# Kernel optimization log

Hardware: AMD Instinct MI355X
Metric: run time of the kernel (lower is better)

## Reference

```python
import jax, jax.numpy as jnp
import numpy as np

N = 20000      # num nodes
E = 320000     # num edges (before self loops)
DIN = 128      # in_channels
DH = 128       # hidden channels
C = 40         # num classes


def setup_inputs() -> dict:
    key = jax.random.key(0)
    ks = jax.random.split(key, 16)
    s_in = 1.0 / np.sqrt(DIN)
    s_h = 1.0 / np.sqrt(DH)
    s_a = 1.0 / np.sqrt(2 * DH)
    return {
        "x": jax.random.normal(ks[0], (N, DIN), jnp.float32),
        "edge_index": jax.random.randint(ks[1], (2, E), 0, N),
        "norm": jax.random.uniform(ks[2], (E + N,), jnp.float32),  # Jaccard sims in [0,1]
        # layer 1 params
        "W1": jax.random.uniform(ks[3], (DIN, DH), jnp.float32, -s_in, s_in),
        "aW1": jax.random.uniform(ks[4], (2 * DH, 1), jnp.float32, -s_a, s_a),
        "ab1": jax.random.uniform(ks[5], (1,), jnp.float32, -s_a, s_a),
        "alpha1": jnp.array([0.5], jnp.float32),
        "b1": jnp.zeros((DH,), jnp.float32),
        # layer 2 params
        "W2": jax.random.uniform(ks[6], (DH, DH), jnp.float32, -s_h, s_h),
        "aW2": jax.random.uniform(ks[7], (2 * DH, 1), jnp.float32, -s_a, s_a),
        "ab2": jax.random.uniform(ks[8], (1,), jnp.float32, -s_a, s_a),
        "alpha2": jnp.array([0.5], jnp.float32),
        "b2": jnp.zeros((DH,), jnp.float32),
        # output head
        "Wout": jax.random.uniform(ks[9], (DH, C), jnp.float32, -s_h, s_h),
        "bout": jax.random.uniform(ks[10], (C,), jnp.float32, -s_h, s_h),
    }


def _gat_layer(x, src, dst, norm, W, aW, ab, alpha, bias):
    n = x.shape[0]
    h = x @ W                              # [N, DH]
    s = h[src]                             # gathered source feats [E', DH]
    t = h[dst]                             # gathered target feats [E', DH]
    # attention logit per edge -> exp(leaky_relu(.))
    e = jnp.exp(jax.nn.leaky_relu(jnp.concatenate([s, t], axis=-1) @ aW + ab,
                                  negative_slope=0.2))          # [E', 1]
    e_sum = jax.ops.segment_sum(e, dst, num_segments=n)         # softmax denom per dst node
    a = e / e_sum[dst]
    s_sim = jnp.exp(norm)[:, None]                               # [E', 1]
    s_sum = jax.ops.segment_sum(s_sim, src, num_segments=n)     # note: summed over SRC (as in original)
    sw = s_sim / s_sum[dst]                                      # but indexed by DST (as in original)
    al = jnp.clip(alpha, 1e-4, 0.9999)
    w = al * a + (1.0 - al) * sw                                 # blended edge weight [E', 1]
    out = jax.ops.segment_max(w * s, dst, num_segments=n)        # aggr='max' propagate
    return out + bias


def reference(x, edge_index, norm, W1, aW1, ab1, alpha1, b1,
              W2, aW2, ab2, alpha2, b2, Wout, bout):
    n = x.shape[0]
    loops = jnp.arange(n, dtype=edge_index.dtype)
    src = jnp.concatenate([edge_index[0], loops])   # add_self_loops
    dst = jnp.concatenate([edge_index[1], loops])
    h = jax.nn.relu(_gat_layer(x, src, dst, norm, W1, aW1, ab1, alpha1, b1))
    h = jax.nn.relu(_gat_layer(h, src, dst, norm, W2, aW2, ab2, alpha2, b2))
    return jax.nn.log_softmax(h @ Wout + bout, axis=-1)
```

## Files before the change

kernel.cpp:

```cpp
#include <hip/hip_runtime.h>
#include <math.h>

#define DHID 128
#define NCLS 40
#define ELLW 64

typedef unsigned int   u32;
typedef unsigned short u16;
using short8 = __attribute__((ext_vector_type(8))) short;
using f32x4  = __attribute__((ext_vector_type(4))) float;

__device__ __forceinline__ u16 f2bf(float f) {
  u32 u = __float_as_uint(f);
  return (u16)((u + 0x7FFFu + ((u >> 16) & 1u)) >> 16);
}
__device__ __forceinline__ float bf_lo(u32 p) { return __uint_as_float(p << 16); }
__device__ __forceinline__ float bf_hi(u32 p) { return __uint_as_float(p & 0xFFFF0000u); }

__global__ __launch_bounds__(256) void prep_kernel(
    const float* __restrict__ x, const float* __restrict__ W1,
    const float* __restrict__ W2, u16* __restrict__ xbf,
    u16* __restrict__ Wp1, u16* __restrict__ Wp2,
    int* __restrict__ counts, float* __restrict__ ssum,
    int* __restrict__ ovf_cnt, int N) {
  int gi = blockIdx.x * 256 + threadIdx.x;
  int Ncvt = N * 16;
  if (gi < Ncvt) {
    int base = gi * 8;
    float4 v0 = *reinterpret_cast<const float4*>(x + base);
    float4 v1 = *reinterpret_cast<const float4*>(x + base + 4);
    uint4 o;
    o.x = (u32)f2bf(v0.x) | ((u32)f2bf(v0.y) << 16);
    o.y = (u32)f2bf(v0.z) | ((u32)f2bf(v0.w) << 16);
    o.z = (u32)f2bf(v1.x) | ((u32)f2bf(v1.y) << 16);
    o.w = (u32)f2bf(v1.z) | ((u32)f2bf(v1.w) << 16);
    *reinterpret_cast<uint4*>(xbf + base) = o;
    return;
  }
  gi -= Ncvt;
  if (gi < N) { counts[gi] = 0; ssum[gi] = 0.f; return; }
  gi -= N;
  if (gi < 32768) {
    int layer = gi >> 14, q = gi & 16383;
    int j = q & 7, l = (q >> 3) & 63, kt = (q >> 9) & 3, ct = q >> 11;
    int k = kt * 32 + (l >> 4) * 8 + j;
    int col = ct * 16 + (l & 15);
    const float* Wsrc = layer ? W2 : W1;
    u16* Wdst = layer ? Wp2 : Wp1;
    Wdst[q] = f2bf(Wsrc[k * DHID + col]);
    return;
  }
  gi -= 32768;
  if (gi == 0) *ovf_cnt = 0;
}

__device__ __forceinline__ void mfma_gemm_block(
    float* Cl, float* P, const u16* __restrict__ Xbf,
    const u16* __restrict__ Wp, const float* __restrict__ aW,
    u16* __restrict__ Hout, float* __restrict__ elo, float* __restrict__ ero,
    int n, int rowBase) {
  int t = threadIdx.x;
  int w = t >> 6, l = t & 63;
  int lr = l & 15, lh = l >> 4;
  f32x4 acc00 = {0.f,0.f,0.f,0.f}, acc01 = {0.f,0.f,0.f,0.f};
  f32x4 acc10 = {0.f,0.f,0.f,0.f}, acc11 = {0.f,0.f,0.f,0.f};
  int r0 = rowBase + lr;      if (r0 > n - 1) r0 = n - 1;
  int r1 = rowBase + 16 + lr; if (r1 > n - 1) r1 = n - 1;
  const u16* a0p = Xbf + (size_t)r0 * DHID;
  const u16* a1p = Xbf + (size_t)r1 * DHID;
  const u16* wb0 = Wp + ((size_t)(w * 2 + 0) * 4 * 64 + l) * 8;
  const u16* wb1 = Wp + ((size_t)(w * 2 + 1) * 4 * 64 + l) * 8;
#pragma unroll
  for (int kt = 0; kt < 4; ++kt) {
    int ko = kt * 32 + lh * 8;
    short8 fa0 = *reinterpret_cast<const short8*>(a0p + ko);
    short8 fa1 = *reinterpret_cast<const short8*>(a1p + ko);
    short8 fb0 = *reinterpret_cast<const short8*>(wb0 + kt * 64 * 8);
    short8 fb1 = *reinterpret_cast<const short8*>(wb1 + kt * 64 * 8);
    acc00 = __builtin_amdgcn_mfma_f32_16x16x32_bf16(fa0, fb0, acc00, 0, 0, 0);
    acc01 = __builtin_amdgcn_mfma_f32_16x16x32_bf16(fa0, fb1, acc01, 0, 0, 0);
    acc10 = __builtin_amdgcn_mfma_f32_16x16x32_bf16(fa1, fb0, acc10, 0, 0, 0);
    acc11 = __builtin_amdgcn_mfma_f32_16x16x32_bf16(fa1, fb1, acc11, 0, 0, 0);
  }
#pragma unroll
  for (int j = 0; j < 4; ++j) {
    Cl[(lh * 4 + j) * DHID + w * 32 + lr]           = acc00[j];
    Cl[(lh * 4 + j) * DHID + w * 32 + 16 + lr]      = acc01[j];
    Cl[(16 + lh * 4 + j) * DHID + w * 32 + lr]      = acc10[j];
    Cl[(16 + lh * 4 + j) * DHID + w * 32 + 16 + lr] = acc11[j];
  }
  __syncthreads();
  int r = t >> 3, cg = (t & 7) * 16;
  const float* crow = Cl + r * DHID + cg;
  float pl = 0.f, pr = 0.f;
  int gr = rowBase + r;
  u32 packed[4];
#pragma unroll
  for (int q = 0; q < 4; ++q) {
    float v0 = crow[q * 4 + 0], v1 = crow[q * 4 + 1];
    float v2 = crow[q * 4 + 2], v3 = crow[q * 4 + 3];
    pl = fmaf(v0, aW[cg + q * 4 + 0], pl); pr = fmaf(v0, aW[DHID + cg + q * 4 + 0], pr);
    pl = fmaf(v1, aW[cg + q * 4 + 1], pl); pr = fmaf(v1, aW[DHID + cg + q * 4 + 1], pr);
    pl = fmaf(v2, aW[cg + q * 4 + 2], pl); pr = fmaf(v2, aW[DHID + cg + q * 4 + 2], pr);
    pl = fmaf(v3, aW[cg + q * 4 + 3], pl); pr = fmaf(v3, aW[DHID + cg + q * 4 + 3], pr);
    packed[q] = (u32)f2bf(v0) | ((u32)f2bf(v1) << 16) |
                0;
    packed[q] |= 0;
  }
  if (gr < n) {
    uint4 o;
    o.x = (u32)f2bf(crow[0])  | ((u32)f2bf(crow[1])  << 16);
    o.y = (u32)f2bf(crow[2])  | ((u32)f2bf(crow[3])  << 16);
    o.z = (u32)f2bf(crow[4])  | ((u32)f2bf(crow[5])  << 16);
    o.w = (u32)f2bf(crow[6])  | ((u32)f2bf(crow[7])  << 16);
    *reinterpret_cast<uint4*>(Hout + (size_t)gr * DHID + cg) = o;
    uint4 o2;
    o2.x = (u32)f2bf(crow[8])  | ((u32)f2bf(crow[9])  << 16);
    o2.y = (u32)f2bf(crow[10]) | ((u32)f2bf(crow[11]) << 16);
    o2.z = (u32)f2bf(crow[12]) | ((u32)f2bf(crow[13]) << 16);
    o2.w = (u32)f2bf(crow[14]) | ((u32)f2bf(crow[15]) << 16);
    *reinterpret_cast<uint4*>(Hout + (size_t)gr * DHID + cg + 8) = o2;
  }
  P[r * 16 + (t & 7) * 2 + 0] = pl;
  P[r * 16 + (t & 7) * 2 + 1] = pr;
  __syncthreads();
  if (t < 64) {
    int half = t >> 5, rr = t & 31;
    float s = 0.f;
#pragma unroll
    for (int cq = 0; cq < 8; ++cq) s += P[rr * 16 + cq * 2 + half];
    int g2 = rowBase + rr;
    if (g2 < n) { if (half) ero[g2] = s; else elo[g2] = s; }
  }
}

__global__ __launch_bounds__(256) void gemm1_build_kernel(
    const u16* __restrict__ Xbf, const u16* __restrict__ Wp,
    const float* __restrict__ aW, u16* __restrict__ H,
    float* __restrict__ el, float* __restrict__ er, int n, int gT,
    const int* __restrict__ ei, const float* __restrict__ norm,
    int* __restrict__ counts, float* __restrict__ ssum,
    uint2* __restrict__ ell, uint4* __restrict__ ovf,
    int* __restrict__ ovf_cnt, int E, int EP) {
  __shared__ float Cl[32 * DHID];
  __shared__ float P[32 * 16];
  if (blockIdx.x < gT) {
    mfma_gemm_block(Cl, P, Xbf, Wp, aW, H, el, er, n, blockIdx.x * 32);
  } else {
    int k = (blockIdx.x - gT) * 256 + threadIdx.x;
    if (k < EP) {
      int src, dst;
      if (k < E) { src = ei[k]; dst = ei[E + k]; }
      else       { src = dst = k - E; }
      float se = __expf(norm[k]);
      atomicAdd(&ssum[src], se);
      int slot = atomicAdd(&counts[dst], 1);
      if (slot < ELLW) {
        ell[(size_t)dst * ELLW + slot] =
            make_uint2((u32)src, __float_as_uint(se));
      } else {
        int o = atomicAdd(ovf_cnt, 1);
        ovf[o] = make_uint4((u32)dst, (u32)src, __float_as_uint(se), 0u);
      }
    }
  }
}

__global__ __launch_bounds__(256) void gemm_elr_kernel(
    const u16* __restrict__ Xbf, const u16* __restrict__ Wp,
    const float* __restrict__ aW, u16* __restrict__ H,
    float* __restrict__ el, float* __restrict__ er, int n) {
  __shared__ float Cl[32 * DHID];
  __shared__ float P[32 * 16];
  mfma_gemm_block(Cl, P, Xbf, Wp, aW, H, el, er, n, blockIdx.x * 32);
}

__device__ __forceinline__ void agg_node8(
    const u16* __restrict__ H, const int* __restrict__ counts,
    const uint2* __restrict__ ell, const uint4* __restrict__ ovf, int ovfN,
    const float* __restrict__ el, const float* __restrict__ ssum,
    float base, float al, int node, int lane, float a[8]) {
  int deg = counts[node];
  int dell = deg < ELLW ? deg : ELLW;
  const uint2* erow = ell + (size_t)node * ELLW;
  int src0 = 0; float sx0 = 0.f;
  if (lane < dell) {
    uint2 rec = erow[lane];
    src0 = (int)rec.x;
    sx0  = __uint_as_float(rec.y);
  }
  int qw = lane >> 4;
  const u16* Hf = H + ((lane & 15) << 3);
  int ei0 = qw, ei1 = 4 + qw;
  int ci0 = ei0 < dell ? ei0 : 0;
  int ci1 = ei1 < dell ? ei1 : 0;
  int ps0 = __shfl(src0, ci0);
  int ps1 = __shfl(src0, ci1);
  uint4 pr0 = *reinterpret_cast<const uint4*>(Hf + (size_t)ps0 * DHID);
  uint4 pr1 = *reinterpret_cast<const uint4*>(Hf + (size_t)ps1 * DHID);
  float e0 = 0.f;
  if (lane < dell) {
    float g = el[src0] + base;
    e0 = __expf(g > 0.f ? g : 0.2f * g);
  }
  float es = e0;
  if (ovfN > 0 && deg > ELLW) {
    for (int cb = 0; cb < ovfN; cb += 64) {
      int i = cb + lane;
      if (i < ovfN) {
        uint4 r = ovf[i];
        if ((int)r.x == node) {
          float g = el[(int)r.y] + base;
          es += __expf(g > 0.f ? g : 0.2f * g);
        }
      }
    }
  }
#pragma unroll
  for (int off = 32; off; off >>= 1) es += __shfl_xor(es, off);
  float invEs = al / es;
  float omaS  = (1.f - al) / ssum[node];
  float w0 = e0 * invEs + sx0 * omaS;
#pragma unroll
  for (int i = 0; i < 8; ++i) a[i] = -INFINITY;
  {
    float wA = __shfl(w0, ci0);
    float wB = __shfl(w0, ci1);
    if (ei0 < dell) {
      a[0] = fmaxf(a[0], wA * bf_lo(pr0.x)); a[1] = fmaxf(a[1], wA * bf_hi(pr0.x));
      a[2] = fmaxf(a[2], wA * bf_lo(pr0.y)); a[3] = fmaxf(a[3], wA * bf_hi(pr0.y));
      a[4] = fmaxf(a[4], wA * bf_lo(pr0.z)); a[5] = fmaxf(a[5], wA * bf_hi(pr0.z));
      a[6] = fmaxf(a[6], wA * bf_lo(pr0.w)); a[7] = fmaxf(a[7], wA * bf_hi(pr0.w));
    }
    if (ei1 < dell) {
      a[0] = fmaxf(a[0], wB * bf_lo(pr1.x)); a[1] = fmaxf(a[1], wB * bf_hi(pr1.x));
      a[2] = fmaxf(a[2], wB * bf_lo(pr1.y)); a[3] = fmaxf(a[3], wB * bf_hi(pr1.y));
      a[4] = fmaxf(a[4], wB * bf_lo(pr1.z)); a[5] = fmaxf(a[5], wB * bf_hi(pr1.z));
      a[6] = fmaxf(a[6], wB * bf_lo(pr1.w)); a[7] = fmaxf(a[7], wB * bf_hi(pr1.w));
    }
  }
  int j = 8;
  for (; j + 7 < dell; j += 8) {
    int ea = j + qw, eb = j + 4 + qw;
    int   sa = __shfl(src0, ea); float wa = __shfl(w0, ea);
    int   sb = __shfl(src0, eb); float wb = __shfl(w0, eb);
    uint4 ha = *reinterpret_cast<const uint4*>(Hf + (size_t)sa * DHID);
    uint4 hb = *reinterpret_cast<const uint4*>(Hf + (size_t)sb * DHID);
    a[0] = fmaxf(a[0], fmaxf(wa * bf_lo(ha.x), wb * bf_lo(hb.x)));
    a[1] = fmaxf(a[1], fmaxf(wa * bf_hi(ha.x), wb * bf_hi(hb.x)));
    a[2] = fmaxf(a[2], fmaxf(wa * bf_lo(ha.y), wb * bf_lo(hb.y)));
    a[3] = fmaxf(a[3], fmaxf(wa * bf_hi(ha.y), wb * bf_hi(hb.y)));
    a[4] = fmaxf(a[4], fmaxf(wa * bf_lo(ha.z), wb * bf_lo(hb.z)));
    a[5] = fmaxf(a[5], fmaxf(wa * bf_hi(ha.z), wb * bf_hi(hb.z)));
    a[6] = fmaxf(a[6], fmaxf(wa * bf_lo(ha.w), wb * bf_lo(hb.w)));
    a[7] = fmaxf(a[7], fmaxf(wa * bf_hi(ha.w), wb * bf_hi(hb.w)));
  }
  for (; j < dell; j += 4) {
    int e = j + qw;
    int ec = e < dell ? e : dell - 1;
    int   sa = __shfl(src0, ec); float wa = __shfl(w0, ec);
    if (e < dell) {
      uint4 ha = *reinterpret_cast<const uint4*>(Hf + (size_t)sa * DHID);
      a[0] = fmaxf(a[0], wa * bf_lo(ha.x));
      a[1] = fmaxf(a[1], wa * bf_hi(ha.x));
      a[2] = fmaxf(a[2], wa * bf_lo(ha.y));
      a[3] = fmaxf(a[3], wa * bf_hi(ha.y));
      a[4] = fmaxf(a[4], wa * bf_lo(ha.z));
      a[5] = fmaxf(a[5], wa * bf_hi(ha.z));
      a[6] = fmaxf(a[6], wa * bf_lo(ha.w));
      a[7] = fmaxf(a[7], wa * bf_hi(ha.w));
    }
  }
  if (ovfN > 0 && deg > ELLW) {
    for (int cb = 0; cb < ovfN; cb += 64) {
      int i = cb + lane;
      uint4 r = (i < ovfN) ? ovf[i] : make_uint4(0u, 0u, 0u, 0u);
      bool match = (i < ovfN) && ((int)r.x == node);
      int si = (int)r.y;
      float wi = 0.f;
      if (match) {
        float g = el[si] + base;
        wi = __expf(g > 0.f ? g : 0.2f * g) * invEs +
             __uint_as_float(r.z) * omaS;
      }
      unsigned long long mask = __ballot(match);
      while (mask) {
        int jb = __ffsll(mask) - 1;
        mask &= mask - 1;
        int   sj = __shfl(si, jb);
        float wj = __shfl(wi, jb);
        uint4 h = *reinterpret_cast<const uint4*>(Hf + (size_t)sj * DHID);
        a[0] = fmaxf(a[0], wj * bf_lo(h.x)); a[1] = fmaxf(a[1], wj * bf_hi(h.x));
        a[2] = fmaxf(a[2], wj * bf_lo(h.y)); a[3] = fmaxf(a[3], wj * bf_hi(h.y));
        a[4] = fmaxf(a[4], wj * bf_lo(h.z)); a[5] = fmaxf(a[5], wj * bf_hi(h.z));
        a[6] = fmaxf(a[6], wj * bf_lo(h.w)); a[7] = fmaxf(a[7], wj * bf_hi(h.w));
      }
    }
  }
#pragma unroll
  for (int i = 0; i < 8; ++i) {
    a[i] = fmaxf(a[i], __shfl_xor(a[i], 16));
    a[i] = fmaxf(a[i], __shfl_xor(a[i], 32));
  }
}

__global__ __launch_bounds__(256) void agg_kernel(
    const u16* __restrict__ H, const int* __restrict__ counts,
    const uint2* __restrict__ ell, const uint4* __restrict__ ovf,
    const int* __restrict__ ovf_cnt, const float* __restrict__ el,
    const float* __restrict__ er, const float* __restrict__ ssum,
    const float* __restrict__ ab, const float* __restrict__ alpha,
    const float* __restrict__ bias, u16* __restrict__ Y, int n) {
  int node = blockIdx.x * 4 + (threadIdx.x >> 6);
  int lane = threadIdx.x & 63;
  if (node >= n) return;
  int ovfN = *ovf_cnt;
  float al = fminf(fmaxf(alpha[0], 1e-4f), 0.9999f);
  float base = er[node] + ab[0];
  float a[8];
  agg_node8(H, counts, ell, ovf, ovfN, el, ssum, base, al, node, lane, a);
  if (lane < 16) {
    int fl = lane << 3;
    float v[8];
#pragma unroll
    for (int i = 0; i < 8; ++i) v[i] = fmaxf(a[i] + bias[fl + i], 0.f);
    uint4 o;
    o.x = (u32)f2bf(v[0]) | ((u32)f2bf(v[1]) << 16);
    o.y = (u32)f2bf(v[2]) | ((u32)f2bf(v[3]) << 16);
    o.z = (u32)f2bf(v[4]) | ((u32)f2bf(v[5]) << 16);
    o.w = (u32)f2bf(v[6]) | ((u32)f2bf(v[7]) << 16);
    *reinterpret_cast<uint4*>(Y + (size_t)node * DHID + fl) = o;
  }
}

__global__ __launch_bounds__(256) void agg_head_kernel(
    const u16* __restrict__ H, const int* __restrict__ counts,
    const uint2* __restrict__ ell, const uint4* __restrict__ ovf,
    const int* __restrict__ ovf_cnt, const float* __restrict__ el,
    const float* __restrict__ er, const float* __restrict__ ssum,
    const float* __restrict__ ab, const float* __restrict__ alpha,
    const float* __restrict__ bias, const float* __restrict__ Wout,
    const float* __restrict__ bout, float* __restrict__ out, int n) {
  __shared__ float Wl[DHID * NCLS];
  __shared__ float hl[4][DHID];
  int t = threadIdx.x;
  for (int i = t; i < DHID * NCLS; i += 256) Wl[i] = Wout[i];
  int wv = t >> 6, lane = t & 63;
  int node = blockIdx.x * 4 + wv;
  if (node < n) {
    int ovfN = *ovf_cnt;
    float al = fminf(fmaxf(alpha[0], 1e-4f), 0.9999f);
    float base = er[node] + ab[0];
    float a[8];
    agg_node8(H, counts, ell, ovf, ovfN, el, ssum, base, al, node, lane, a);
    if (lane < 16) {
      int fl = lane << 3;
#pragma unroll
      for (int i = 0; i < 8; ++i)
        hl[wv][fl + i] = fmaxf(a[i] + bias[fl + i], 0.f);
    }
  }
  __syncthreads();
  if (node >= n) return;
  float z = -INFINITY;
  bool act = lane < NCLS;
  if (act) {
    z = bout[lane];
    const float* hr = hl[wv];
#pragma unroll 8
    for (int k = 0; k < DHID; ++k) z = fmaf(hr[k], Wl[k * NCLS + lane], z);
  }
  float m = z;
#pragma unroll
  for (int off = 32; off; off >>= 1) m = fmaxf(m, __shfl_xor(m, off));
  float p = act ? expf(z - m) : 0.f;
#pragma unroll
  for (int off = 32; off; off >>= 1) p += __shfl_xor(p, off);
  float ls = logf(p);
  if (act) out[(size_t)node * NCLS + lane] = z - m - ls;
}

extern "C" void kernel_launch(void* const* d_in, const int* in_sizes, int n_in,
                              void* d_out, int out_size, void* d_ws, size_t ws_size,
                              hipStream_t stream) {
  const float* x     = (const float*)d_in[0];
  const int*   ei    = (const int*)d_in[1];
  const float* norm  = (const float*)d_in[2];
  const float* W1    = (const float*)d_in[3];
  const float* aW1   = (const float*)d_in[4];
  const float* ab1   = (const float*)d_in[5];
  const float* alpha1= (const float*)d_in[6];
  const float* b1    = (const float*)d_in[7];
  const float* W2    = (const float*)d_in[8];
  const float* aW2   = (const float*)d_in[9];
  const float* ab2   = (const float*)d_in[10];
  const float* alpha2= (const float*)d_in[11];
  const float* b2    = (const float*)d_in[12];
  const float* Wout  = (const float*)d_in[13];
  const float* bout  = (const float*)d_in[14];
  float* out = (float*)d_out;

  const int N  = in_sizes[0] / DHID;
  const int E  = in_sizes[1] / 2;
  const int EP = E + N;

  char* ws = (char*)d_ws;
  size_t off = 0;
  auto alloc = [&](size_t bytes) -> void* {
    void* p = ws + off;
    off += (bytes + 255) & ~(size_t)255;
    return p;
  };
  int*   counts  = (int*)  alloc((size_t)N * 4);
  float* ssum    = (float*)alloc((size_t)N * 4);
  int*   ovf_cnt = (int*)  alloc(256);
  u16*   xbf     = (u16*)  alloc((size_t)N * DHID * 2);
  u16*   Wp1     = (u16*)  alloc(16384 * 2);
  u16*   Wp2     = (u16*)  alloc(16384 * 2);
  u16*   Hbf     = (u16*)  alloc((size_t)N * DHID * 2);
  u16*   Bbf     = (u16*)  alloc((size_t)N * DHID * 2);
  float* el      = (float*)alloc((size_t)N * 4);
  float* er      = (float*)alloc((size_t)N * 4);
  uint2* ell     = (uint2*)alloc((size_t)N * ELLW * 8);
  uint4* ovf     = (uint4*)alloc((size_t)EP * 16);

  const int gEdge = (EP + 255) / 256;
  const int gT    = (N + 31) / 32;
  const int gAgg  = (N + 3) / 4;
  const int prepWork = N * 16 + N + 32768 + 1;
  const int gPrep = (prepWork + 255) / 256;

  prep_kernel<<<gPrep, 256, 0, stream>>>(x, W1, W2, xbf, Wp1, Wp2,
                                         counts, ssum, ovf_cnt, N);
  gemm1_build_kernel<<<gT + gEdge, 256, 0, stream>>>(
      xbf, Wp1, aW1, Hbf, el, er, N, gT, ei, norm, counts, ssum, ell, ovf,
      ovf_cnt, E, EP);
  agg_kernel<<<gAgg, 256, 0, stream>>>(Hbf, counts, ell, ovf, ovf_cnt, el, er,
                                       ssum, ab1, alpha1, b1, Bbf, N);
  gemm_elr_kernel<<<gT, 256, 0, stream>>>(Bbf, Wp2, aW2, Hbf, el, er, N);
  agg_head_kernel<<<gAgg, 256, 0, stream>>>(Hbf, counts, ell, ovf, ovf_cnt,
                                            el, er, ssum, ab2, alpha2, b2,
                                            Wout, bout, out, N);
}
```

Measured before the change: 104.7 us.

## Fuse all stages into one cooperative persistent kernel with grid syncs

```diff
diff --git a/kernel.cpp b/kernel.cpp
--- a/kernel.cpp
+++ b/kernel.cpp
@@ -1,9 +1,12 @@
 #include <hip/hip_runtime.h>
+#include <hip/hip_cooperative_groups.h>
 #include <math.h>
 
 #define DHID 128
 #define NCLS 40
 #define ELLW 64
+
+namespace cg = cooperative_groups;
 
 typedef unsigned int   u32;
 typedef unsigned short u16;
@@ -17,48 +20,26 @@
 __device__ __forceinline__ float bf_lo(u32 p) { return __uint_as_float(p << 16); }
 __device__ __forceinline__ float bf_hi(u32 p) { return __uint_as_float(p & 0xFFFF0000u); }
 
-__global__ __launch_bounds__(256) void prep_kernel(
-    const float* __restrict__ x, const float* __restrict__ W1,
-    const float* __restrict__ W2, u16* __restrict__ xbf,
-    u16* __restrict__ Wp1, u16* __restrict__ Wp2,
-    int* __restrict__ counts, float* __restrict__ ssum,
-    int* __restrict__ ovf_cnt, int N) {
-  int gi = blockIdx.x * 256 + threadIdx.x;
-  int Ncvt = N * 16;
-  if (gi < Ncvt) {
-    int base = gi * 8;
-    float4 v0 = *reinterpret_cast<const float4*>(x + base);
-    float4 v1 = *reinterpret_cast<const float4*>(x + base + 4);
-    uint4 o;
-    o.x = (u32)f2bf(v0.x) | ((u32)f2bf(v0.y) << 16);
-    o.y = (u32)f2bf(v0.z) | ((u32)f2bf(v0.w) << 16);
-    o.z = (u32)f2bf(v1.x) | ((u32)f2bf(v1.y) << 16);
-    o.w = (u32)f2bf(v1.z) | ((u32)f2bf(v1.w) << 16);
-    *reinterpret_cast<uint4*>(xbf + base) = o;
-    return;
-  }
-  gi -= Ncvt;
-  if (gi < N) { counts[gi] = 0; ssum[gi] = 0.f; return; }
-  gi -= N;
-  if (gi < 32768) {
-    int layer = gi >> 14, q = gi & 16383;
-    int j = q & 7, l = (q >> 3) & 63, kt = (q >> 9) & 3, ct = q >> 11;
-    int k = kt * 32 + (l >> 4) * 8 + j;
-    int col = ct * 16 + (l & 15);
-    const float* Wsrc = layer ? W2 : W1;
-    u16* Wdst = layer ? Wp2 : Wp1;
-    Wdst[q] = f2bf(Wsrc[k * DHID + col]);
-    return;
-  }
-  gi -= 32768;
-  if (gi == 0) *ovf_cnt = 0;
-}
-
+__device__ __forceinline__ short8 packbf(float4 a, float4 b) {
+  short8 r;
+  r[0] = (short)f2bf(a.x); r[1] = (short)f2bf(a.y);
+  r[2] = (short)f2bf(a.z); r[3] = (short)f2bf(a.w);
+  r[4] = (short)f2bf(b.x); r[5] = (short)f2bf(b.y);
+  r[6] = (short)f2bf(b.z); r[7] = (short)f2bf(b.w);
+  return r;
+}
+
+union SharedU {
+  struct { float Cl[32 * DHID]; float P[32 * 16]; } g;
+  struct { float Wl[DHID * NCLS]; float hl[4][DHID]; } h;
+};
+
+template <bool BF16IN>
 __device__ __forceinline__ void mfma_gemm_block(
-    float* Cl, float* P, const u16* __restrict__ Xbf,
-    const u16* __restrict__ Wp, const float* __restrict__ aW,
-    u16* __restrict__ Hout, float* __restrict__ elo, float* __restrict__ ero,
-    int n, int rowBase) {
+    float* Cl, float* P, const float* __restrict__ Xf,
+    const u16* __restrict__ Xh, const u16* __restrict__ Wp,
+    const float* __restrict__ aW, u16* __restrict__ Hout,
+    float* __restrict__ elo, float* __restrict__ ero, int n, int rowBase) {
   int t = threadIdx.x;
   int w = t >> 6, l = t & 63;
   int lr = l & 15, lh = l >> 4;
@@ -66,15 +47,23 @@
   f32x4 acc10 = {0.f,0.f,0.f,0.f}, acc11 = {0.f,0.f,0.f,0.f};
   int r0 = rowBase + lr;      if (r0 > n - 1) r0 = n - 1;
   int r1 = rowBase + 16 + lr; if (r1 > n - 1) r1 = n - 1;
-  const u16* a0p = Xbf + (size_t)r0 * DHID;
-  const u16* a1p = Xbf + (size_t)r1 * DHID;
   const u16* wb0 = Wp + ((size_t)(w * 2 + 0) * 4 * 64 + l) * 8;
   const u16* wb1 = Wp + ((size_t)(w * 2 + 1) * 4 * 64 + l) * 8;
 #pragma unroll
   for (int kt = 0; kt < 4; ++kt) {
     int ko = kt * 32 + lh * 8;
-    short8 fa0 = *reinterpret_cast<const short8*>(a0p + ko);
-    short8 fa1 = *reinterpret_cast<const short8*>(a1p + ko);
+    short8 fa0, fa1;
+    if constexpr (BF16IN) {
+      fa0 = *reinterpret_cast<const short8*>(Xh + (size_t)r0 * DHID + ko);
+      fa1 = *reinterpret_cast<const short8*>(Xh + (size_t)r1 * DHID + ko);
+    } else {
+      const float* a0f = Xf + (size_t)r0 * DHID + ko;
+      const float* a1f = Xf + (size_t)r1 * DHID + ko;
+      fa0 = packbf(*reinterpret_cast<const float4*>(a0f),
+                   *reinterpret_cast<const float4*>(a0f + 4));
+      fa1 = packbf(*reinterpret_cast<const float4*>(a1f),
+                   *reinterpret_cast<const float4*>(a1f + 4));
+    }
     short8 fb0 = *reinterpret_cast<const short8*>(wb0 + kt * 64 * 8);
     short8 fb1 = *reinterpret_cast<const short8*>(wb1 + kt * 64 * 8);
     acc00 = __builtin_amdgcn_mfma_f32_16x16x32_bf16(fa0, fb0, acc00, 0, 0, 0);
@@ -90,22 +79,15 @@
     Cl[(16 + lh * 4 + j) * DHID + w * 32 + 16 + lr] = acc11[j];
   }
   __syncthreads();
-  int r = t >> 3, cg = (t & 7) * 16;
-  const float* crow = Cl + r * DHID + cg;
+  int r = t >> 3, cg2 = (t & 7) * 16;
+  const float* crow = Cl + r * DHID + cg2;
   float pl = 0.f, pr = 0.f;
   int gr = rowBase + r;
-  u32 packed[4];
-#pragma unroll
-  for (int q = 0; q < 4; ++q) {
-    float v0 = crow[q * 4 + 0], v1 = crow[q * 4 + 1];
-    float v2 = crow[q * 4 + 2], v3 = crow[q * 4 + 3];
-    pl = fmaf(v0, aW[cg + q * 4 + 0], pl); pr = fmaf(v0, aW[DHID + cg + q * 4 + 0], pr);
-    pl = fmaf(v1, aW[cg + q * 4 + 1], pl); pr = fmaf(v1, aW[DHID + cg + q * 4 + 1], pr);
-    pl = fmaf(v2, aW[cg + q * 4 + 2], pl); pr = fmaf(v2, aW[DHID + cg + q * 4 + 2], pr);
-    pl = fmaf(v3, aW[cg + q * 4 + 3], pl); pr = fmaf(v3, aW[DHID + cg + q * 4 + 3], pr);
-    packed[q] = (u32)f2bf(v0) | ((u32)f2bf(v1) << 16) |
-                0;
-    packed[q] |= 0;
+#pragma unroll
+  for (int q = 0; q < 16; ++q) {
+    float v = crow[q];
+    pl = fmaf(v, aW[cg2 + q], pl);
+    pr = fmaf(v, aW[DHID + cg2 + q], pr);
   }
   if (gr < n) {
     uint4 o;
@@ -113,13 +95,13 @@
     o.y = (u32)f2bf(crow[2])  | ((u32)f2bf(crow[3])  << 16);
     o.z = (u32)f2bf(crow[4])  | ((u32)f2bf(crow[5])  << 16);
     o.w = (u32)f2bf(crow[6])  | ((u32)f2bf(crow[7])  << 16);
-    *reinterpret_cast<uint4*>(Hout + (size_t)gr * DHID + cg) = o;
+    *reinterpret_cast<uint4*>(Hout + (size_t)gr * DHID + cg2) = o;
     uint4 o2;
     o2.x = (u32)f2bf(crow[8])  | ((u32)f2bf(crow[9])  << 16);
     o2.y = (u32)f2bf(crow[10]) | ((u32)f2bf(crow[11]) << 16);
     o2.z = (u32)f2bf(crow[12]) | ((u32)f2bf(crow[13]) << 16);
     o2.w = (u32)f2bf(crow[14]) | ((u32)f2bf(crow[15]) << 16);
-    *reinterpret_cast<uint4*>(Hout + (size_t)gr * DHID + cg + 8) = o2;
+    *reinterpret_cast<uint4*>(Hout + (size_t)gr * DHID + cg2 + 8) = o2;
   }
   P[r * 16 + (t & 7) * 2 + 0] = pl;
   P[r * 16 + (t & 7) * 2 + 1] = pr;
@@ -132,47 +114,6 @@
     int g2 = rowBase + rr;
     if (g2 < n) { if (half) ero[g2] = s; else elo[g2] = s; }
   }
-}
-
-__global__ __launch_bounds__(256) void gemm1_build_kernel(
-    const u16* __restrict__ Xbf, const u16* __restrict__ Wp,
-    const float* __restrict__ aW, u16* __restrict__ H,
-    float* __restrict__ el, float* __restrict__ er, int n, int gT,
-    const int* __restrict__ ei, const float* __restrict__ norm,
-    int* __restrict__ counts, float* __restrict__ ssum,
-    uint2* __restrict__ ell, uint4* __restrict__ ovf,
-    int* __restrict__ ovf_cnt, int E, int EP) {
-  __shared__ float Cl[32 * DHID];
-  __shared__ float P[32 * 16];
-  if (blockIdx.x < gT) {
-    mfma_gemm_block(Cl, P, Xbf, Wp, aW, H, el, er, n, blockIdx.x * 32);
-  } else {
-    int k = (blockIdx.x - gT) * 256 + threadIdx.x;
-    if (k < EP) {
-      int src, dst;
-      if (k < E) { src = ei[k]; dst = ei[E + k]; }
-      else       { src = dst = k - E; }
-      float se = __expf(norm[k]);
-      atomicAdd(&ssum[src], se);
-      int slot = atomicAdd(&counts[dst], 1);
-      if (slot < ELLW) {
-        ell[(size_t)dst * ELLW + slot] =
-            make_uint2((u32)src, __float_as_uint(se));
-      } else {
-        int o = atomicAdd(ovf_cnt, 1);
-        ovf[o] = make_uint4((u32)dst, (u32)src, __float_as_uint(se), 0u);
-      }
-    }
-  }
-}
-
-__global__ __launch_bounds__(256) void gemm_elr_kernel(
-    const u16* __restrict__ Xbf, const u16* __restrict__ Wp,
-    const float* __restrict__ aW, u16* __restrict__ H,
-    float* __restrict__ el, float* __restrict__ er, int n) {
-  __shared__ float Cl[32 * DHID];
-  __shared__ float P[32 * 16];
-  mfma_gemm_block(Cl, P, Xbf, Wp, aW, H, el, er, n, blockIdx.x * 32);
 }
 
 __device__ __forceinline__ void agg_node8(
@@ -304,80 +245,144 @@
   }
 }
 
-__global__ __launch_bounds__(256) void agg_kernel(
-    const u16* __restrict__ H, const int* __restrict__ counts,
-    const uint2* __restrict__ ell, const uint4* __restrict__ ovf,
-    const int* __restrict__ ovf_cnt, const float* __restrict__ el,
-    const float* __restrict__ er, const float* __restrict__ ssum,
-    const float* __restrict__ ab, const float* __restrict__ alpha,
-    const float* __restrict__ bias, u16* __restrict__ Y, int n) {
-  int node = blockIdx.x * 4 + (threadIdx.x >> 6);
-  int lane = threadIdx.x & 63;
-  if (node >= n) return;
-  int ovfN = *ovf_cnt;
-  float al = fminf(fmaxf(alpha[0], 1e-4f), 0.9999f);
-  float base = er[node] + ab[0];
-  float a[8];
-  agg_node8(H, counts, ell, ovf, ovfN, el, ssum, base, al, node, lane, a);
-  if (lane < 16) {
-    int fl = lane << 3;
-    float v[8];
-#pragma unroll
-    for (int i = 0; i < 8; ++i) v[i] = fmaxf(a[i] + bias[fl + i], 0.f);
-    uint4 o;
-    o.x = (u32)f2bf(v[0]) | ((u32)f2bf(v[1]) << 16);
-    o.y = (u32)f2bf(v[2]) | ((u32)f2bf(v[3]) << 16);
-    o.z = (u32)f2bf(v[4]) | ((u32)f2bf(v[5]) << 16);
-    o.w = (u32)f2bf(v[6]) | ((u32)f2bf(v[7]) << 16);
-    *reinterpret_cast<uint4*>(Y + (size_t)node * DHID + fl) = o;
-  }
-}
-
-__global__ __launch_bounds__(256) void agg_head_kernel(
-    const u16* __restrict__ H, const int* __restrict__ counts,
-    const uint2* __restrict__ ell, const uint4* __restrict__ ovf,
-    const int* __restrict__ ovf_cnt, const float* __restrict__ el,
-    const float* __restrict__ er, const float* __restrict__ ssum,
-    const float* __restrict__ ab, const float* __restrict__ alpha,
-    const float* __restrict__ bias, const float* __restrict__ Wout,
-    const float* __restrict__ bout, float* __restrict__ out, int n) {
-  __shared__ float Wl[DHID * NCLS];
-  __shared__ float hl[4][DHID];
+__global__ __launch_bounds__(256) void mega_kernel(
+    const float* __restrict__ x, const int* __restrict__ ei,
+    const float* __restrict__ norm,
+    const float* __restrict__ W1, const float* __restrict__ aW1,
+    const float* __restrict__ ab1, const float* __restrict__ alpha1,
+    const float* __restrict__ b1,
+    const float* __restrict__ W2, const float* __restrict__ aW2,
+    const float* __restrict__ ab2, const float* __restrict__ alpha2,
+    const float* __restrict__ b2,
+    const float* __restrict__ Wout, const float* __restrict__ bout,
+    float* __restrict__ out,
+    int* counts, float* ssum, int* ovf_cnt,
+    u16* Wp1, u16* Wp2, u16* Hbf, u16* Bbf,
+    float* el, float* er, uint2* ell, uint4* ovf,
+    int N, int E, int EP, int gT, int gEdge, int gAgg) {
+  cg::grid_group grid = cg::this_grid();
+  __shared__ SharedU sh;
   int t = threadIdx.x;
-  for (int i = t; i < DHID * NCLS; i += 256) Wl[i] = Wout[i];
-  int wv = t >> 6, lane = t & 63;
-  int node = blockIdx.x * 4 + wv;
-  if (node < n) {
+  int stride = gridDim.x * 256;
+
+  for (int i = blockIdx.x * 256 + t; i < N; i += stride) {
+    counts[i] = 0; ssum[i] = 0.f;
+  }
+  for (int q = blockIdx.x * 256 + t; q < 32768; q += stride) {
+    int layer = q >> 14, qq = q & 16383;
+    int j = qq & 7, l = (qq >> 3) & 63, kt = (qq >> 9) & 3, ct = qq >> 11;
+    int k = kt * 32 + (l >> 4) * 8 + j;
+    int col = ct * 16 + (l & 15);
+    (layer ? Wp2 : Wp1)[qq] = f2bf((layer ? W2 : W1)[k * DHID + col]);
+  }
+  if (blockIdx.x == 0 && t == 0) *ovf_cnt = 0;
+  grid.sync();
+
+  {
+    int work = gT + gEdge;
+    for (int wb = blockIdx.x; wb < work; wb += gridDim.x) {
+      if (wb < gT) {
+        mfma_gemm_block<false>(sh.g.Cl, sh.g.P, x, nullptr, Wp1, aW1, Hbf,
+                               el, er, N, wb * 32);
+      } else {
+        int k = (wb - gT) * 256 + t;
+        if (k < EP) {
+          int src, dst;
+          if (k < E) { src = ei[k]; dst = ei[E + k]; }
+          else       { src = dst = k - E; }
+          float se = __expf(norm[k]);
+          atomicAdd(&ssum[src], se);
+          int slot = atomicAdd(&counts[dst], 1);
+          if (slot < ELLW) {
+            ell[(size_t)dst * ELLW + slot] =
+                make_uint2((u32)src, __float_as_uint(se));
+          } else {
+            int o = atomicAdd(ovf_cnt, 1);
+            ovf[o] = make_uint4((u32)dst, (u32)src, __float_as_uint(se), 0u);
+          }
+        }
+      }
+    }
+  }
+  grid.sync();
+
+  {
     int ovfN = *ovf_cnt;
-    float al = fminf(fmaxf(alpha[0], 1e-4f), 0.9999f);
-    float base = er[node] + ab[0];
-    float a[8];
-    agg_node8(H, counts, ell, ovf, ovfN, el, ssum, base, al, node, lane, a);
-    if (lane < 16) {
-      int fl = lane << 3;
-#pragma unroll
-      for (int i = 0; i < 8; ++i)
-        hl[wv][fl + i] = fmaxf(a[i] + bias[fl + i], 0.f);
-    }
-  }
-  __syncthreads();
-  if (node >= n) return;
-  float z = -INFINITY;
-  bool act = lane < NCLS;
-  if (act) {
-    z = bout[lane];
-    const float* hr = hl[wv];
+    float al = fminf(fmaxf(alpha1[0], 1e-4f), 0.9999f);
+    float abv = ab1[0];
+    int lane = t & 63, wv = t >> 6;
+    for (int wb = blockIdx.x; wb < gAgg; wb += gridDim.x) {
+      int node = wb * 4 + wv;
+      if (node < N) {
+        float base = er[node] + abv;
+        float a[8];
+        agg_node8(Hbf, counts, ell, ovf, ovfN, el, ssum, base, al, node, lane, a);
+        if (lane < 16) {
+          int fl = lane << 3;
+          float v[8];
+#pragma unroll
+          for (int i = 0; i < 8; ++i) v[i] = fmaxf(a[i] + b1[fl + i], 0.f);
+          uint4 o;
+          o.x = (u32)f2bf(v[0]) | ((u32)f2bf(v[1]) << 16);
+          o.y = (u32)f2bf(v[2]) | ((u32)f2bf(v[3]) << 16);
+          o.z = (u32)f2bf(v[4]) | ((u32)f2bf(v[5]) << 16);
+          o.w = (u32)f2bf(v[6]) | ((u32)f2bf(v[7]) << 16);
+          *reinterpret_cast<uint4*>(Bbf + (size_t)node * DHID + fl) = o;
+        }
+      }
+    }
+  }
+  grid.sync();
+
+  for (int wb = blockIdx.x; wb < gT; wb += gridDim.x) {
+    mfma_gemm_block<true>(sh.g.Cl, sh.g.P, nullptr, Bbf, Wp2, aW2, Hbf,
+                          el, er, N, wb * 32);
+  }
+  grid.sync();
+
+  {
+    for (int i = t; i < DHID * NCLS; i += 256) sh.h.Wl[i] = Wout[i];
+    __syncthreads();
+    int ovfN = *ovf_cnt;
+    float al = fminf(fmaxf(alpha2[0], 1e-4f), 0.9999f);
+    float abv = ab2[0];
+    int lane = t & 63, wv = t >> 6;
+    for (int wb = blockIdx.x; wb < gAgg; wb += gridDim.x) {
+      int node = wb * 4 + wv;
+      if (node < N) {
+        float base = er[node] + abv;
+        float a[8];
+        agg_node8(Hbf, counts, ell, ovf, ovfN, el, ssum, base, al, node, lane, a);
+        if (lane < 16) {
+          int fl = lane << 3;
+#pragma unroll
+          for (int i = 0; i < 8; ++i)
+            sh.h.hl[wv][fl + i] = fmaxf(a[i] + b2[fl + i], 0.f);
+        }
+      }
+      __syncthreads();
+      if (node < N) {
+        float z = -INFINITY;
+        bool act = lane < NCLS;
+        if (act) {
+          z = bout[lane];
+          const float* hr = sh.h.hl[wv];
 #pragma unroll 8
-    for (int k = 0; k < DHID; ++k) z = fmaf(hr[k], Wl[k * NCLS + lane], z);
-  }
-  float m = z;
-#pragma unroll
-  for (int off = 32; off; off >>= 1) m = fmaxf(m, __shfl_xor(m, off));
-  float p = act ? expf(z - m) : 0.f;
-#pragma unroll
-  for (int off = 32; off; off >>= 1) p += __shfl_xor(p, off);
-  float ls = logf(p);
-  if (act) out[(size_t)node * NCLS + lane] = z - m - ls;
+          for (int k = 0; k < DHID; ++k)
+            z = fmaf(hr[k], sh.h.Wl[k * NCLS + lane], z);
+        }
+        float m = z;
+#pragma unroll
+        for (int off = 32; off; off >>= 1) m = fmaxf(m, __shfl_xor(m, off));
+        float p = act ? expf(z - m) : 0.f;
+#pragma unroll
+        for (int off = 32; off; off >>= 1) p += __shfl_xor(p, off);
+        float ls = logf(p);
+        if (act) out[(size_t)node * NCLS + lane] = z - m - ls;
+      }
+      __syncthreads();
+    }
+  }
 }
 
 extern "C" void kernel_launch(void* const* d_in, const int* in_sizes, int n_in,
@@ -400,9 +405,9 @@
   const float* bout  = (const float*)d_in[14];
   float* out = (float*)d_out;
 
-  const int N  = in_sizes[0] / DHID;
-  const int E  = in_sizes[1] / 2;
-  const int EP = E + N;
+  int N  = in_sizes[0] / DHID;
+  int E  = in_sizes[1] / 2;
+  int EP = E + N;
 
   char* ws = (char*)d_ws;
   size_t off = 0;
@@ -414,7 +419,6 @@
   int*   counts  = (int*)  alloc((size_t)N * 4);
   float* ssum    = (float*)alloc((size_t)N * 4);
   int*   ovf_cnt = (int*)  alloc(256);
-  u16*   xbf     = (u16*)  alloc((size_t)N * DHID * 2);
   u16*   Wp1     = (u16*)  alloc(16384 * 2);
   u16*   Wp2     = (u16*)  alloc(16384 * 2);
   u16*   Hbf     = (u16*)  alloc((size_t)N * DHID * 2);
@@ -424,21 +428,32 @@
   uint2* ell     = (uint2*)alloc((size_t)N * ELLW * 8);
   uint4* ovf     = (uint4*)alloc((size_t)EP * 16);
 
-  const int gEdge = (EP + 255) / 256;
-  const int gT    = (N + 31) / 32;
-  const int gAgg  = (N + 3) / 4;
-  const int prepWork = N * 16 + N + 32768 + 1;
-  const int gPrep = (prepWork + 255) / 256;
-
-  prep_kernel<<<gPrep, 256, 0, stream>>>(x, W1, W2, xbf, Wp1, Wp2,
-                                         counts, ssum, ovf_cnt, N);
-  gemm1_build_kernel<<<gT + gEdge, 256, 0, stream>>>(
-      xbf, Wp1, aW1, Hbf, el, er, N, gT, ei, norm, counts, ssum, ell, ovf,
-      ovf_cnt, E, EP);
-  agg_kernel<<<gAgg, 256, 0, stream>>>(Hbf, counts, ell, ovf, ovf_cnt, el, er,
-                                       ssum, ab1, alpha1, b1, Bbf, N);
-  gemm_elr_kernel<<<gT, 256, 0, stream>>>(Bbf, Wp2, aW2, Hbf, el, er, N);
-  agg_head_kernel<<<gAgg, 256, 0, stream>>>(Hbf, counts, ell, ovf, ovf_cnt,
-                                            el, er, ssum, ab2, alpha2, b2,
-                                            Wout, bout, out, N);
-}
+  int gT    = (N + 31) / 32;
+  int gEdge = (EP + 255) / 256;
+  int gAgg  = (N + 3) / 4;
+
+  int devCU = 256;
+  hipDeviceProp_t prop;
+  if (hipGetDeviceProperties(&prop, 0) == hipSuccess &&
+      prop.multiProcessorCount > 0)
+    devCU = prop.multiProcessorCount;
+  int perCU = 0;
+  hipOccupancyMaxActiveBlocksPerMultiprocessor(&perCU, mega_kernel, 256, 0);
+  if (perCU < 1) perCU = 1;
+  long long nbl = (long long)perCU * devCU;
+  if (nbl > 2048) nbl = 2048;
+  int NB = (int)nbl;
+
+  void* args[] = {
+    (void*)&x, (void*)&ei, (void*)&norm,
+    (void*)&W1, (void*)&aW1, (void*)&ab1, (void*)&alpha1, (void*)&b1,
+    (void*)&W2, (void*)&aW2, (void*)&ab2, (void*)&alpha2, (void*)&b2,
+    (void*)&Wout, (void*)&bout, (void*)&out,
+    (void*)&counts, (void*)&ssum, (void*)&ovf_cnt,
+    (void*)&Wp1, (void*)&Wp2, (void*)&Hbf, (void*)&Bbf,
+    (void*)&el, (void*)&er, (void*)&ell, (void*)&ovf,
+    (void*)&N, (void*)&E, (void*)&EP, (void*)&gT, (void*)&gEdge, (void*)&gAgg
+  };
+  hipLaunchCooperativeKernel((const void*)mega_kernel, dim3(NB), dim3(256),
+                             args, 0, stream);
+}
```

After: 375.4 us. 3.58x slower.
